# Kernel optimization log

Measured on AMD Instinct MI355X. Metric: run time of the kernel, lower is better.

## Reference

```python
import jax, jax.numpy as jnp
import numpy as np

L, H, E, HS, T, B, V = 6, 12, 768, 64, 1024, 2, 32000
EPS = 1e-5


def layer_norm(x, g, b):
    mu = jnp.mean(x, axis=-1, keepdims=True)
    var = jnp.mean(jnp.square(x - mu), axis=-1, keepdims=True)
    return (x - mu) * jax.lax.rsqrt(var + EPS) * g + b


def setup_inputs() -> dict:
    key = jax.random.key(0)
    ks = jax.random.split(key, 24)
    s = 0.02
    inp = {
        "idx": jax.random.randint(ks[0], (B, T), 0, V),
        "targets": jax.random.randint(ks[1], (B, T), 0, V),
        "tok_emb": jax.random.normal(ks[2], (V, E), jnp.float32) * s,
        "pos_emb": jax.random.normal(ks[3], (T, E), jnp.float32) * s,
        "ln1_g": jnp.ones((L, E), jnp.float32),
        "ln1_b": jnp.zeros((L, E), jnp.float32),
        "wq": jax.random.normal(ks[4], (L, E, E), jnp.float32) * s,
        "wk": jax.random.normal(ks[5], (L, E, E), jnp.float32) * s,
        "wv": jax.random.normal(ks[6], (L, E, E), jnp.float32) * s,
        "wproj": jax.random.normal(ks[7], (L, E, E), jnp.float32) * s,
        "bproj": jnp.zeros((L, E), jnp.float32),
        "ln2_g": jnp.ones((L, E), jnp.float32),
        "ln2_b": jnp.zeros((L, E), jnp.float32),
        "w1": jax.random.normal(ks[8], (L, E, 4 * E), jnp.float32) * s,
        "b1": jnp.zeros((L, 4 * E), jnp.float32),
        "w2": jax.random.normal(ks[9], (L, 4 * E, E), jnp.float32) * s,
        "b2": jnp.zeros((L, E), jnp.float32),
        "lnf_g": jnp.ones((E,), jnp.float32),
        "lnf_b": jnp.zeros((E,), jnp.float32),
        "lm_w": jax.random.normal(ks[10], (E, V), jnp.float32) * s,
        "lm_b": jnp.zeros((V,), jnp.float32),
    }
    return inp


def reference(idx, targets, tok_emb, pos_emb, ln1_g, ln1_b, wq, wk, wv, wproj,
              bproj, ln2_g, ln2_b, w1, b1, w2, b2, lnf_g, lnf_b, lm_w, lm_b):
    x = tok_emb[idx] + pos_emb[None, :T, :]  # [B,T,E]
    causal = jnp.tril(jnp.ones((T, T), bool))
    scale = E ** (-0.5)  # NOTE: original scales by n_embed**-0.5, not head_size
    for l in range(L):
        h = layer_norm(x, ln1_g[l], ln1_b[l])
        q = (h @ wq[l]).reshape(B, T, H, HS)
        k = (h @ wk[l]).reshape(B, T, H, HS)
        v = (h @ wv[l]).reshape(B, T, H, HS)
        scores = jnp.einsum('bqhd,bkhd->bhqk', q, k) * scale
        scores = jnp.where(causal[None, None], scores, -jnp.inf)
        w = jax.nn.softmax(scores, axis=-1)
        attn = jnp.einsum('bhqk,bkhd->bqhd', w, v).reshape(B, T, E)
        # original MultiHeadAttention applies proj TWICE (faithful reproduction)
        out = attn @ wproj[l] + bproj[l]
        out = out @ wproj[l] + bproj[l]
        x = x + out
        h2 = layer_norm(x, ln2_g[l], ln2_b[l])
        x = x + (jax.nn.relu(h2 @ w1[l] + b1[l]) @ w2[l] + b2[l])
    x = layer_norm(x, lnf_g, lnf_b)
    logits = x @ lm_w + lm_b  # [B,T,V]
    logp = jax.nn.log_softmax(logits, axis=-1)
    nll = -jnp.take_along_axis(logp, targets[..., None], axis=-1)[..., 0]
    loss = jnp.mean(nll)
    return logits, loss
```

## Files before the change

kernel.cpp:

```cpp
#include <hip/hip_runtime.h>
#include <math.h>

#define NL 6
#define NH 12
#define NE 768
#define NHS 64
#define NT 1024
#define NB 2
#define NV 32000
#define NM (NB * NT)
#define NQKV (3 * NE)
#define NFF (4 * NE)
#define LN_EPS 1e-5f

typedef __attribute__((ext_vector_type(8))) short short8;
typedef __attribute__((ext_vector_type(4))) float f32x4;
typedef __attribute__((ext_vector_type(4))) unsigned short ushort4v;
typedef __attribute__((address_space(1))) const unsigned int as1_cuint;
typedef __attribute__((address_space(3))) unsigned int as3_uint;

__device__ __forceinline__ unsigned short f2bf(float f) {
    unsigned int u = __builtin_bit_cast(unsigned int, f);
    u += 0x7fffu + ((u >> 16) & 1u);
    return (unsigned short)(u >> 16);
}
__device__ __forceinline__ float bf2f(unsigned short u) {
    unsigned int v = ((unsigned int)u) << 16;
    return __builtin_bit_cast(float, v);
}
__device__ __forceinline__ void gload_lds16(const void* g, void* l) {
    __builtin_amdgcn_global_load_lds((as1_cuint*)g, (as3_uint*)l, 16, 0, 0);
}

__global__ __launch_bounds__(256) void embed_ln_kernel(const int* __restrict__ idx,
                                                       const float* __restrict__ tok,
                                                       const float* __restrict__ pos,
                                                       const float* __restrict__ g,
                                                       const float* __restrict__ b,
                                                       float* __restrict__ x,
                                                       unsigned short* __restrict__ hbuf) {
    __shared__ float red[256];
    int row = blockIdx.x, tid = threadIdx.x;
    int t = row % NT;
    int id = idx[row];
    float v[3]; float s = 0.f;
    #pragma unroll
    for (int k = 0; k < 3; ++k) {
        int c = tid + k * 256;
        v[k] = tok[(long)id * NE + c] + pos[(long)t * NE + c];
        x[(long)row * NE + c] = v[k];
        s += v[k];
    }
    red[tid] = s; __syncthreads();
    for (int o = 128; o > 0; o >>= 1) { if (tid < o) red[tid] += red[tid + o]; __syncthreads(); }
    float mu = red[0] / NE;
    __syncthreads();
    float vr = 0.f;
    #pragma unroll
    for (int k = 0; k < 3; ++k) { float d = v[k] - mu; vr += d * d; }
    red[tid] = vr; __syncthreads();
    for (int o = 128; o > 0; o >>= 1) { if (tid < o) red[tid] += red[tid + o]; __syncthreads(); }
    float rstd = rsqrtf(red[0] / NE + LN_EPS);
    #pragma unroll
    for (int k = 0; k < 3; ++k) {
        int c = tid + k * 256;
        hbuf[(long)row * NE + c] = f2bf((v[k] - mu) * rstd * g[c] + b[c]);
    }
}

template<int S>
__global__ __launch_bounds__(256) void combine_ln_kernel(const float* __restrict__ parts,
                                                         const float* __restrict__ bias,
                                                         float* __restrict__ x,
                                                         const float* __restrict__ g,
                                                         const float* __restrict__ b,
                                                         unsigned short* __restrict__ hbuf) {
    __shared__ float red[256];
    int row = blockIdx.x, tid = threadIdx.x;
    float v[3]; float s = 0.f;
    #pragma unroll
    for (int k = 0; k < 3; ++k) {
        int c = tid + k * 256;
        long i = (long)row * NE + c;
        float a = parts[i];
        #pragma unroll
        for (int si = 1; si < S; ++si) a += parts[(long)si * NM * NE + i];
        a += bias[c] + x[i];
        x[i] = a;
        v[k] = a; s += a;
    }
    red[tid] = s; __syncthreads();
    for (int o = 128; o > 0; o >>= 1) { if (tid < o) red[tid] += red[tid + o]; __syncthreads(); }
    float mu = red[0] / NE;
    __syncthreads();
    float vr = 0.f;
    #pragma unroll
    for (int k = 0; k < 3; ++k) { float d = v[k] - mu; vr += d * d; }
    red[tid] = vr; __syncthreads();
    for (int o = 128; o > 0; o >>= 1) { if (tid < o) red[tid] += red[tid + o]; __syncthreads(); }
    float rstd = rsqrtf(red[0] / NE + LN_EPS);
    #pragma unroll
    for (int k = 0; k < 3; ++k) {
        int c = tid + k * 256;
        hbuf[(long)row * NE + c] = f2bf((v[k] - mu) * rstd * g[c] + b[c]);
    }
}

__global__ __launch_bounds__(256) void transpose4b_kernel(const float* __restrict__ wq,
                                                          const float* __restrict__ wk,
                                                          const float* __restrict__ wv,
                                                          const float* __restrict__ wp,
                                                          unsigned short* __restrict__ wqkvT,
                                                          unsigned short* __restrict__ wprojT) {
    __shared__ float t[32][33];
    int z = blockIdx.z, l = z >> 2, which = z & 3;
    const float* W = ((which == 0) ? wq : (which == 1) ? wk : (which == 2) ? wv : wp) + (long)l * NE * NE;
    unsigned short* WT = (which < 3) ? (wqkvT + (long)l * NQKV * NE + (long)which * NE * NE)
                                     : (wprojT + (long)l * NE * NE);
    int k0 = blockIdx.y * 32, n0 = blockIdx.x * 32;
    int c = threadIdx.x & 31, r = threadIdx.x >> 5;
    #pragma unroll
    for (int p = 0; p < 4; ++p)
        t[r + p * 8][c] = W[(long)(k0 + r + p * 8) * NE + n0 + c];
    __syncthreads();
    #pragma unroll
    for (int p = 0; p < 4; ++p)
        WT[(long)(n0 + r + p * 8) * NE + k0 + c] = f2bf(t[c][r + p * 8]);
}

__global__ __launch_bounds__(256) void transpose_cast_b_kernel(const float* __restrict__ W0,
                                                               unsigned short* __restrict__ WT0,
                                                               int K, int N) {
    __shared__ float t[32][33];
    long lofs = (long)blockIdx.z * K * N;
    const float* W = W0 + lofs;
    unsigned short* WT = WT0 + lofs;
    int k0 = blockIdx.y * 32, n0 = blockIdx.x * 32;
    int c = threadIdx.x & 31, r = threadIdx.x >> 5;
    #pragma unroll
    for (int p = 0; p < 4; ++p)
        t[r + p * 8][c] = W[(long)(k0 + r + p * 8) * N + n0 + c];
    __syncthreads();
    #pragma unroll
    for (int p = 0; p < 4; ++p)
        WT[(long)(n0 + r + p * 8) * K + k0 + c] = f2bf(t[c][r + p * 8]);
}

__global__ __launch_bounds__(256) void cast_kernel(const float* __restrict__ W,
                                                   unsigned short* __restrict__ O, long n) {
    long i = ((long)blockIdx.x * 256 + threadIdx.x) * 4;
    if (i < n) {
        float4 v = *(const float4*)(W + i);
        ushort4v o;
        o[0] = f2bf(v.x); o[1] = f2bf(v.y); o[2] = f2bf(v.z); o[3] = f2bf(v.w);
        *(ushort4v*)(O + i) = o;
    }
}

__global__ __launch_bounds__(256) void beff_b_kernel(const float* __restrict__ bproj,
                                                     const unsigned short* __restrict__ wprojT,
                                                     float* __restrict__ beff) {
    __shared__ float red[256];
    int n = blockIdx.x, l = blockIdx.y, tid = threadIdx.x;
    const unsigned short* wp = wprojT + (long)l * NE * NE + (long)n * NE;
    const float* bp = bproj + (long)l * NE;
    float acc = 0.f;
    for (int j = tid; j < NE; j += 256) acc += bp[j] * bf2f(wp[j]);
    red[tid] = acc; __syncthreads();
    for (int o = 128; o > 0; o >>= 1) { if (tid < o) red[tid] += red[tid + o]; __syncthreads(); }
    if (tid == 0) beff[(long)l * NE + n] = red[0] + bp[n];
}

template<int S>
__global__ __launch_bounds__(256) void combine_kernel(const float* __restrict__ parts,
                                                      unsigned short* __restrict__ bout,
                                                      long total) {
    long i = ((long)blockIdx.x * 256 + threadIdx.x) * 4;
    if (i >= total) return;
    float4 a = *(const float4*)(parts + i);
    #pragma unroll
    for (int s = 1; s < S; ++s) {
        float4 b = *(const float4*)(parts + (long)s * total + i);
        a.x += b.x; a.y += b.y; a.z += b.z; a.w += b.w;
    }
    ushort4v o;
    o[0] = f2bf(a.x); o[1] = f2bf(a.y); o[2] = f2bf(a.z); o[3] = f2bf(a.w);
    *(ushort4v*)(bout + i) = o;
}

template<typename OutT, bool BIAS, bool RELU, int SPLITK>
__global__ __launch_bounds__(256) void gemm_mfma(const unsigned short* __restrict__ A,
                                                 const unsigned short* __restrict__ BT,
                                                 const float* __restrict__ bias,
                                                 OutT* __restrict__ C,
                                                 int gridM, int N, int K) {
    __shared__ unsigned short As[3][128 * 32];
    __shared__ unsigned short Bs[3][128 * 32];
    int tid = threadIdx.x;
    int lane = tid & 63, w = tid >> 6;
    int wr = w >> 1, wc = w & 1;
    int l4 = lane >> 4, l15 = lane & 15;

    int nwg = gridDim.x, orig = blockIdx.x;
    int q = nwg >> 3, r8 = nwg & 7;
    int xcd = orig & 7, ii = orig >> 3;
    int wg = (xcd < r8) ? (xcd * (q + 1) + ii) : (r8 * (q + 1) + (xcd - r8) * q + ii);
    int bm = wg % gridM, bn = wg / gridM;
    int m0 = bm * 128, n0 = bn * 128;

    int kb = K / SPLITK;
    int koff = (SPLITK > 1) ? blockIdx.y * kb : 0;
    int nkt = kb >> 5;

    f32x4 acc[4][4] = {};

    int srow = lane >> 2;
    int scol = ((lane & 3) ^ ((lane >> 3) & 3)) * 8;
    int rsw  = (l4 ^ ((l15 >> 1) & 3)) * 8;

    auto STAGE = [&](int slot, int kt) {
        #pragma unroll
        for (int it = 0; it < 2; ++it) {
            int rr = w * 32 + it * 16;
            gload_lds16(&A [(long)(m0 + rr + srow) * K + koff + kt * 32 + scol], &As[slot][rr * 32]);
            gload_lds16(&BT[(long)(n0 + rr + srow) * K + koff + kt * 32 + scol], &Bs[slot][rr * 32]);
        }
    };

    STAGE(0, 0);
    if (nkt > 1) STAGE(1, 1);

    int s = 0;
    for (int t = 0; t < nkt; ++t) {
        if (t + 2 < nkt) STAGE((t + 2) % 3, t + 2);
        int ahead = nkt - 1 - t;
        if (ahead >= 2)      asm volatile("s_waitcnt vmcnt(8)" ::: "memory");
        else if (ahead == 1) asm volatile("s_waitcnt vmcnt(4)" ::: "memory");
        else                 asm volatile("s_waitcnt vmcnt(0)" ::: "memory");
        asm volatile("s_barrier" ::: "memory");

        short8 a[4], b[4];
        #pragma unroll
        for (int f = 0; f < 4; ++f) {
            a[f] = *(const short8*)&As[s][(wr * 64 + f * 16 + l15) * 32 + rsw];
            b[f] = *(const short8*)&Bs[s][(wc * 64 + f * 16 + l15) * 32 + rsw];
        }
        asm volatile("s_waitcnt lgkmcnt(0)" ::: "memory");
        asm volatile("s_barrier" ::: "memory");

        __builtin_amdgcn_s_setprio(1);
        #pragma unroll
        for (int fm = 0; fm < 4; ++fm)
            #pragma unroll
            for (int fn = 0; fn < 4; ++fn)
                acc[fm][fn] = __builtin_amdgcn_mfma_f32_16x16x32_bf16(a[fm], b[fn], acc[fm][fn], 0, 0, 0);
        __builtin_amdgcn_s_setprio(0);
        s = (s + 1) % 3;
    }

    if constexpr (SPLITK > 1) {
        float* Cp = (float*)C + (long)blockIdx.y * gridM * 128 * N;
        #pragma unroll
        for (int fm = 0; fm < 4; ++fm)
            #pragma unroll
            for (int j = 0; j < 4; ++j) {
                long row = m0 + wr * 64 + fm * 16 + l4 * 4 + j;
                #pragma unroll
                for (int fn = 0; fn < 4; ++fn)
                    Cp[row * N + n0 + wc * 64 + fn * 16 + l15] = acc[fm][fn][j];
            }
    } else {
        float bs[4];
        #pragma unroll
        for (int fn = 0; fn < 4; ++fn)
            bs[fn] = BIAS ? bias[n0 + wc * 64 + fn * 16 + l15] : 0.f;

        #pragma unroll
        for (int fm = 0; fm < 4; ++fm) {
            #pragma unroll
            for (int j = 0; j < 4; ++j) {
                long row = m0 + wr * 64 + fm * 16 + l4 * 4 + j;
                #pragma unroll
                for (int fn = 0; fn < 4; ++fn) {
                    int col = n0 + wc * 64 + fn * 16 + l15;
                    float v = acc[fm][fn][j] + bs[fn];
                    if (RELU) v = fmaxf(v, 0.f);
                    if constexpr (sizeof(OutT) == 2) C[row * N + col] = (OutT)f2bf(v);
                    else                             C[row * N + col] = v;
                }
            }
        }
    }
}

__global__ __launch_bounds__(256) void gemm_weff_kernel(const unsigned short* __restrict__ A0,
                                                        const unsigned short* __restrict__ B0,
                                                        unsigned short* __restrict__ C0,
                                                        int gridM, int N, int K) {
    __shared__ unsigned short As[2][128 * 32];
    __shared__ unsigned short Bs[2][128 * 32];
    long zofs = (long)blockIdx.z * N * K;
    const unsigned short* A = A0 + zofs;
    const unsigned short* BT = B0 + zofs;
    unsigned short* C = C0 + zofs;
    int tid = threadIdx.x;
    int lane = tid & 63, w = tid >> 6;
    int wr = w >> 1, wc = w & 1;
    int l4 = lane >> 4, l15 = lane & 15;
    int bm = blockIdx.x % gridM, bn = blockIdx.x / gridM;
    int m0 = bm * 128, n0 = bn * 128;

    f32x4 acc[4][4] = {};
    int srow = lane >> 2;
    int scol = ((lane & 3) ^ ((lane >> 3) & 3)) * 8;
    int rsw  = (l4 ^ ((l15 >> 1) & 3)) * 8;

    #pragma unroll
    for (int it = 0; it < 2; ++it) {
        int rr = w * 32 + it * 16;
        gload_lds16(&A [(long)(m0 + rr + srow) * K + scol], &As[0][rr * 32]);
        gload_lds16(&BT[(long)(n0 + rr + srow) * K + scol], &Bs[0][rr * 32]);
    }
    int cur = 0;
    for (int k0 = 0; k0 < K; k0 += 32) {
        __syncthreads();
        if (k0 + 32 < K) {
            #pragma unroll
            for (int it = 0; it < 2; ++it) {
                int rr = w * 32 + it * 16;
                gload_lds16(&A [(long)(m0 + rr + srow) * K + k0 + 32 + scol], &As[cur ^ 1][rr * 32]);
                gload_lds16(&BT[(long)(n0 + rr + srow) * K + k0 + 32 + scol], &Bs[cur ^ 1][rr * 32]);
            }
        }
        short8 a[4], b[4];
        #pragma unroll
        for (int f = 0; f < 4; ++f) {
            a[f] = *(const short8*)&As[cur][(wr * 64 + f * 16 + l15) * 32 + rsw];
            b[f] = *(const short8*)&Bs[cur][(wc * 64 + f * 16 + l15) * 32 + rsw];
        }
        #pragma unroll
        for (int fm = 0; fm < 4; ++fm)
            #pragma unroll
            for (int fn = 0; fn < 4; ++fn)
                acc[fm][fn] = __builtin_amdgcn_mfma_f32_16x16x32_bf16(a[fm], b[fn], acc[fm][fn], 0, 0, 0);
        cur ^= 1;
    }
    #pragma unroll
    for (int fm = 0; fm < 4; ++fm)
        #pragma unroll
        for (int j = 0; j < 4; ++j) {
            long row = m0 + wr * 64 + fm * 16 + l4 * 4 + j;
            #pragma unroll
            for (int fn = 0; fn < 4; ++fn)
                C[row * N + n0 + wc * 64 + fn * 16 + l15] = f2bf(acc[fm][fn][j]);
        }
}

__global__ __launch_bounds__(512, 4) void gemm256x128_lse(const unsigned short* __restrict__ A,
                                                          const unsigned short* __restrict__ BT,
                                                          const float* __restrict__ bias,
                                                          float* __restrict__ C,
                                                          float* __restrict__ pm, float* __restrict__ ps,
                                                          int gridM, int N, int K) {
    __shared__ unsigned short Al[3][256 * 32];
    __shared__ unsigned short Bl[3][128 * 32];
    int tid = threadIdx.x;
    int lane = tid & 63, w = tid >> 6;
    int wm = w >> 1, wn = w & 1;
    int l4 = lane >> 4, l15 = lane & 15;

    int nwg = gridDim.x, orig = blockIdx.x;
    int q = nwg >> 3, r8 = nwg & 7;
    int xcd = orig & 7, ii = orig >> 3;
    int wg = (xcd < r8) ? (xcd * (q + 1) + ii) : (r8 * (q + 1) + (xcd - r8) * q + ii);
    int bm = wg % gridM, bn = wg / gridM;
    int m0 = bm * 256, n0 = bn * 128;

    int nkt = K >> 5;
    int srow = lane >> 2;
    int sslot = ((lane & 3) ^ ((lane >> 3) & 3)) * 8;

    auto STAGE = [&](int slot, int kt) {
        #pragma unroll
        for (int p = 0; p < 2; ++p) {
            int r0 = p * 128 + w * 16;
            gload_lds16(&A[(long)(m0 + r0 + srow) * K + kt * 32 + sslot], &Al[slot][r0 * 32]);
        }
        int r0 = w * 16;
        gload_lds16(&BT[(long)(n0 + r0 + srow) * K + kt * 32 + sslot], &Bl[slot][r0 * 32]);
    };

    f32x4 acc[4][4] = {};
    int rsw = (l4 ^ ((l15 >> 1) & 3)) * 8;

    STAGE(0, 0);
    STAGE(1, 1);
    int s = 0;
    for (int t = 0; t < nkt; ++t) {
        if (t + 2 < nkt) STAGE((t + 2) % 3, t + 2);
        int ahead = nkt - 1 - t;
        if (ahead >= 2)      asm volatile("s_waitcnt vmcnt(6)" ::: "memory");
        else if (ahead == 1) asm volatile("s_waitcnt vmcnt(3)" ::: "memory");
        else                 asm volatile("s_waitcnt vmcnt(0)" ::: "memory");
        asm volatile("s_barrier" ::: "memory");

        short8 af[4], bf[4];
        #pragma unroll
        for (int f = 0; f < 4; ++f) {
            af[f] = *(const short8*)&Al[s][(wm * 64 + f * 16 + l15) * 32 + rsw];
            bf[f] = *(const short8*)&Bl[s][(wn * 64 + f * 16 + l15) * 32 + rsw];
        }
        asm volatile("s_waitcnt lgkmcnt(0)" ::: "memory");
        asm volatile("s_barrier" ::: "memory");

        __builtin_amdgcn_s_setprio(1);
        #pragma unroll
        for (int fm = 0; fm < 4; ++fm)
            #pragma unroll
            for (int fn = 0; fn < 4; ++fn)
                acc[fm][fn] = __builtin_amdgcn_mfma_f32_16x16x32_bf16(af[fm], bf[fn], acc[fm][fn], 0, 0, 0);
        __builtin_amdgcn_s_setprio(0);
        s = (s + 1) % 3;
    }

    float bs[4];
    #pragma unroll
    for (int fn = 0; fn < 4; ++fn)
        bs[fn] = bias[n0 + wn * 64 + fn * 16 + l15];

    #pragma unroll
    for (int fm = 0; fm < 4; ++fm) {
        #pragma unroll
        for (int j = 0; j < 4; ++j) {
            long row = m0 + wm * 64 + fm * 16 + l4 * 4 + j;
            float v4[4];
            #pragma unroll
            for (int fn = 0; fn < 4; ++fn) {
                int col = n0 + wn * 64 + fn * 16 + l15;
                float v = acc[fm][fn][j] + bs[fn];
                __builtin_nontemporal_store(v, &C[row * N + col]);
                v4[fn] = v;
            }
            float mx = fmaxf(fmaxf(v4[0], v4[1]), fmaxf(v4[2], v4[3]));
            #pragma unroll
            for (int off = 1; off < 16; off <<= 1) mx = fmaxf(mx, __shfl_xor(mx, off));
            float sm = 0.f;
            #pragma unroll
            for (int fn = 0; fn < 4; ++fn) sm += __expf(v4[fn] - mx);
            #pragma unroll
            for (int off = 1; off < 16; off <<= 1) sm += __shfl_xor(sm, off);
            if (l15 == 0) {
                int pidx = bn * 2 + wn;
                pm[row * 512 + pidx] = mx;
                ps[row * 512 + pidx] = sm;
            }
        }
    }
}

__global__ __launch_bounds__(256) void vtrans_kernel(const unsigned short* __restrict__ qkv,
                                                     unsigned short* __restrict__ vt) {
    __shared__ unsigned short t[64][72];
    int t0 = blockIdx.x * 64;
    int bh = blockIdx.y;
    int b = bh / NH, h = bh % NH;
    int tid = threadIdx.x;
    #pragma unroll
    for (int i = 0; i < 2; ++i) {
        int r = (tid >> 3) + i * 32, c8 = (tid & 7) * 8;
        short8 v = *(const short8*)(qkv + ((long)b * NT + t0 + r) * NQKV + 2 * NE + h * NHS + c8);
        *(short8*)&t[r][c8] = v;
    }
    __syncthreads();
    #pragma unroll
    for (int i = 0; i < 2; ++i) {
        int d = (tid >> 3) + i * 32, s = (tid & 7) * 8;
        short8 o;
        #pragma unroll
        for (int j = 0; j < 8; ++j) o[j] = (short)t[s + j][d];
        *(short8*)(vt + ((long)bh * NHS + d) * NT + t0 + s) = o;
    }
}

__global__ __launch_bounds__(256) void fattn_kernel(const unsigned short* __restrict__ qkv,
                                                    const unsigned short* __restrict__ vt,
                                                    unsigned short* __restrict__ out) {
    __shared__ unsigned short Ks[2][64 * 64];
    __shared__ unsigned short Vl[2][64 * 64];
    __shared__ unsigned short Ps[4 * 16 * 64];
    int qt = gridDim.x - 1 - blockIdx.x;
    int bh = blockIdx.y;
    int b = bh / NH, h = bh % NH;
    int tid = threadIdx.x, lane = tid & 63, w = tid >> 6;
    int l4 = lane >> 4, l15 = lane & 15;
    long rowb = (long)b * NT;
    const float scale = 0.03608439182435161f;
    const unsigned short* vtp = vt + (long)bh * NHS * NT;

    const unsigned short* qptr = qkv + (rowb + qt * 64 + w * 16 + l15) * NQKV + h * NHS;
    short8 qa0 = *(const short8*)(qptr + l4 * 8);
    short8 qa1 = *(const short8*)(qptr + 32 + l4 * 8);

    f32x4 o[4] = {};
    float m[4], lsum[4];
    #pragma unroll
    for (int j = 0; j < 4; ++j) { m[j] = -INFINITY; lsum[j] = 0.f; }

    int kr_r = tid >> 3, kr_c = (tid & 7) * 8;
    int vr_d = tid >> 3, vr_s = tid & 7;

    short8 kr[2], vr[2];
    auto LOADT = [&](int t) {
        int kbase = t * 64;
        #pragma unroll
        for (int i = 0; i < 2; ++i) {
            kr[i] = *(const short8*)(qkv + (rowb + kbase + kr_r + i * 32) * NQKV + NE + h * NHS + kr_c);
            vr[i] = *(const short8*)(vtp + (long)(vr_d + i * 32) * NT + kbase + vr_s * 8);
        }
    };

    LOADT(0);
    for (int t = 0; t <= qt; ++t) {
        int cur = t & 1;
        #pragma unroll
        for (int i = 0; i < 2; ++i) {
            int r = kr_r + i * 32;
            *(short8*)&Ks[cur][r * 64 + (kr_c ^ ((r & 7) << 3))] = kr[i];
            int d = vr_d + i * 32;
            *(short8*)&Vl[cur][d * 64 + ((vr_s * 8) ^ ((d & 7) << 3))] = vr[i];
        }
        asm volatile("s_waitcnt lgkmcnt(0)" ::: "memory");
        if (t < qt) LOADT(t + 1);
        asm volatile("s_barrier" ::: "memory");

        f32x4 s[4];
        __builtin_amdgcn_s_setprio(1);
        #pragma unroll
        for (int fn = 0; fn < 4; ++fn) {
            int key = fn * 16 + l15;
            short8 kb0 = *(const short8*)&Ks[cur][key * 64 + ((l4 * 8) ^ ((key & 7) << 3))];
            short8 kb1 = *(const short8*)&Ks[cur][key * 64 + ((32 + l4 * 8) ^ ((key & 7) << 3))];
            f32x4 z = {};
            z = __builtin_amdgcn_mfma_f32_16x16x32_bf16(qa0, kb0, z, 0, 0, 0);
            s[fn] = __builtin_amdgcn_mfma_f32_16x16x32_bf16(qa1, kb1, z, 0, 0, 0);
        }
        __builtin_amdgcn_s_setprio(0);

        if (t == qt) {
            #pragma unroll
            for (int fn = 0; fn < 4; ++fn) {
                int key = t * 64 + fn * 16 + l15;
                #pragma unroll
                for (int j = 0; j < 4; ++j) {
                    int qrow = qt * 64 + w * 16 + l4 * 4 + j;
                    s[fn][j] = (key <= qrow) ? s[fn][j] * scale : -1e30f;
                }
            }
        } else {
            #pragma unroll
            for (int fn = 0; fn < 4; ++fn)
                #pragma unroll
                for (int j = 0; j < 4; ++j)
                    s[fn][j] *= scale;
        }

        #pragma unroll
        for (int j = 0; j < 4; ++j) {
            float mj = fmaxf(fmaxf(s[0][j], s[1][j]), fmaxf(s[2][j], s[3][j]));
            #pragma unroll
            for (int off = 1; off < 16; off <<= 1) mj = fmaxf(mj, __shfl_xor(mj, off));
            float mnew = fmaxf(m[j], mj);
            float alpha = __expf(m[j] - mnew);
            m[j] = mnew;
            float psum = 0.f;
            #pragma unroll
            for (int fn = 0; fn < 4; ++fn) {
                float p = __expf(s[fn][j] - mnew);
                psum += p;
                int rr = l4 * 4 + j, c = fn * 16 + l15;
                Ps[w * 1024 + rr * 64 + (c ^ ((rr & 7) << 3))] = f2bf(p);
            }
            #pragma unroll
            for (int off = 1; off < 16; off <<= 1) psum += __shfl_xor(psum, off);
            lsum[j] = lsum[j] * alpha + psum;
            #pragma unroll
            for (int fn = 0; fn < 4; ++fn) o[fn][j] *= alpha;
        }

        short8 pa0 = *(const short8*)&Ps[w * 1024 + l15 * 64 + ((l4 * 8) ^ ((l15 & 7) << 3))];
        short8 pa1 = *(const short8*)&Ps[w * 1024 + l15 * 64 + ((32 + l4 * 8) ^ ((l15 & 7) << 3))];
        __builtin_amdgcn_s_setprio(1);
        #pragma unroll
        for (int fn = 0; fn < 4; ++fn) {
            int d = fn * 16 + l15;
            short8 vb0 = *(const short8*)&Vl[cur][d * 64 + ((l4 * 8) ^ ((d & 7) << 3))];
            short8 vb1 = *(const short8*)&Vl[cur][d * 64 + ((32 + l4 * 8) ^ ((d & 7) << 3))];
            o[fn] = __builtin_amdgcn_mfma_f32_16x16x32_bf16(pa0, vb0, o[fn], 0, 0, 0);
            o[fn] = __builtin_amdgcn_mfma_f32_16x16x32_bf16(pa1, vb1, o[fn], 0, 0, 0);
        }
        __builtin_amdgcn_s_setprio(0);
    }

    #pragma unroll
    for (int j = 0; j < 4; ++j) {
        long row = rowb + qt * 64 + w * 16 + l4 * 4 + j;
        float inv = 1.0f / lsum[j];
        #pragma unroll
        for (int fn = 0; fn < 4; ++fn)
            out[row * NE + h * NHS + fn * 16 + l15] = f2bf(o[fn][j] * inv);
    }
}

__global__ __launch_bounds__(256) void nll_combine_kernel(const float* __restrict__ logits,
                                                          const float* __restrict__ pm,
                                                          const float* __restrict__ ps,
                                                          const int* __restrict__ targets,
                                                          float* __restrict__ nll) {
    __shared__ float rm[256], rs[256];
    int row = blockIdx.x, tid = threadIdx.x;
    float m = -1e30f, s = 0.f;
    for (int i = tid; i < 500; i += 256) {
        float m2 = pm[(long)row * 512 + i], s2 = ps[(long)row * 512 + i];
        float mm = fmaxf(m, m2);
        s = s * __expf(m - mm) + s2 * __expf(m2 - mm);
        m = mm;
    }
    rm[tid] = m; rs[tid] = s; __syncthreads();
    for (int o = 128; o > 0; o >>= 1) {
        if (tid < o) {
            float m2 = rm[tid + o], s2 = rs[tid + o];
            float mm = fmaxf(rm[tid], m2);
            rs[tid] = rs[tid] * __expf(rm[tid] - mm) + s2 * __expf(m2 - mm);
            rm[tid] = mm;
        }
        __syncthreads();
    }
    if (tid == 0) {
        int tgt = targets[row];
        nll[row] = -(logits[(long)row * NV + tgt] - rm[0] - logf(rs[0]));
    }
}

__global__ void loss_reduce_kernel(const float* __restrict__ nll, float* __restrict__ out) {
    __shared__ float red[256];
    int tid = threadIdx.x;
    float s = 0.f;
    for (int i = tid; i < NM; i += 256) s += nll[i];
    red[tid] = s; __syncthreads();
    for (int o = 128; o > 0; o >>= 1) { if (tid < o) red[tid] += red[tid + o]; __syncthreads(); }
    if (tid == 0) out[0] = red[0] / NM;
}

extern "C" void kernel_launch(void* const* d_in, const int* in_sizes, int n_in,
                              void* d_out, int out_size, void* d_ws, size_t ws_size,
                              hipStream_t stream) {
    const int*   idx     = (const int*)  d_in[0];
    const int*   targets = (const int*)  d_in[1];
    const float* tok     = (const float*)d_in[2];
    const float* pos     = (const float*)d_in[3];
    const float* ln1_g   = (const float*)d_in[4];
    const float* ln1_b   = (const float*)d_in[5];
    const float* wq      = (const float*)d_in[6];
    const float* wk      = (const float*)d_in[7];
    const float* wv      = (const float*)d_in[8];
    const float* wproj   = (const float*)d_in[9];
    const float* bproj   = (const float*)d_in[10];
    const float* ln2_g   = (const float*)d_in[11];
    const float* ln2_b   = (const float*)d_in[12];
    const float* w1      = (const float*)d_in[13];
    const float* b1      = (const float*)d_in[14];
    const float* w2      = (const float*)d_in[15];
    const float* b2      = (const float*)d_in[16];
    const float* lnf_g   = (const float*)d_in[17];
    const float* lnf_b   = (const float*)d_in[18];
    const float* lm_w    = (const float*)d_in[19];
    const float* lm_b    = (const float*)d_in[20];

    float* logits = (float*)d_out;
    float* loss   = logits + (long)NM * NV;

    char* p = (char*)d_ws;
    float*          x      = (float*)p;          p += (long)NM * NE * 4;
    unsigned short* hbuf   = (unsigned short*)p; p += (long)NM * NE * 2;
    unsigned short* qkv    = (unsigned short*)p; p += (long)NM * NQKV * 2;
    unsigned short* att    = (unsigned short*)p; p += (long)NM * NE * 2;
    unsigned short* hid    = (unsigned short*)p; p += (long)NM * NFF * 2;
    unsigned short* vt     = (unsigned short*)p; p += (long)NB * NH * NHS * NT * 2;
    float*          nll    = (float*)p;          p += (long)NM * 4;
    float*          pmb    = (float*)p;          p += (long)NM * 512 * 4;
    float*          psb    = (float*)p;          p += (long)NM * 512 * 4;
    float*          parts  = (float*)p;          p += (long)2 * NM * NQKV * 4;
    unsigned short* wqkvT6 = (unsigned short*)p; p += (long)NL * NQKV * NE * 2;
    unsigned short* wprojT6= (unsigned short*)p; p += (long)NL * NE * NE * 2;
    unsigned short* wprojC6= (unsigned short*)p; p += (long)NL * NE * NE * 2;
    unsigned short* weffT6 = (unsigned short*)p; p += (long)NL * NE * NE * 2;
    float*          beff6  = (float*)p;          p += (long)NL * NE * 4;
    unsigned short* w1T6   = (unsigned short*)p; p += (long)NL * NFF * NE * 2;
    unsigned short* w2T6   = (unsigned short*)p; p += (long)NL * NE * NFF * 2;
    unsigned short* lmT    = (unsigned short*)p; p += (long)NV * NE * 2;

    dim3 blk(256);

    transpose4b_kernel<<<dim3(NE / 32, NE / 32, 4 * NL), blk, 0, stream>>>(
        wq, wk, wv, wproj, wqkvT6, wprojT6);
    cast_kernel<<<(NL * NE * NE) / 1024, blk, 0, stream>>>(wproj, wprojC6, (long)NL * NE * NE);
    transpose_cast_b_kernel<<<dim3(NFF / 32, NE / 32, NL), blk, 0, stream>>>(w1, w1T6, NE, NFF);
    transpose_cast_b_kernel<<<dim3(NE / 32, NFF / 32, NL), blk, 0, stream>>>(w2, w2T6, NFF, NE);
    gemm_weff_kernel<<<dim3(36, 1, NL), blk, 0, stream>>>(wprojT6, wprojC6, weffT6, 6, NE, NE);
    beff_b_kernel<<<dim3(NE, NL), blk, 0, stream>>>(bproj, wprojT6, beff6);
    transpose_cast_b_kernel<<<dim3(NV / 32, NE / 32, 1), blk, 0, stream>>>(lm_w, lmT, NE, NV);

    embed_ln_kernel<<<NM, blk, 0, stream>>>(idx, tok, pos, ln1_g, ln1_b, x, hbuf);

    for (int l = 0; l < NL; ++l) {
        gemm_mfma<float, false, false, 2><<<dim3((NM/128)*(NQKV/128), 2), blk, 0, stream>>>(
            hbuf, wqkvT6 + (long)l * NQKV * NE, nullptr, parts, NM / 128, NQKV, NE);
        combine_kernel<2><<<(NM * NQKV) / 1024, blk, 0, stream>>>(parts, qkv, (long)NM * NQKV);
        vtrans_kernel<<<dim3(NT / 64, NB * NH), blk, 0, stream>>>(qkv, vt);
        fattn_kernel<<<dim3(NT / 64, NB * NH), blk, 0, stream>>>(qkv, vt, att);
        gemm_mfma<float, false, false, 2><<<dim3((NM/128)*(NE/128), 2), blk, 0, stream>>>(
            att, weffT6 + (long)l * NE * NE, nullptr, parts, NM / 128, NE, NE);
        combine_ln_kernel<2><<<NM, blk, 0, stream>>>(
            parts, beff6 + (long)l * NE, x, ln2_g + (long)l * NE, ln2_b + (long)l * NE, hbuf);
        gemm_mfma<unsigned short, true, true, 1><<<dim3((NM/128)*(NFF/128)), blk, 0, stream>>>(
            hbuf, w1T6 + (long)l * NFF * NE, b1 + (long)l * NFF, hid, NM / 128, NFF, NE);
        gemm_mfma<float, false, false, 4><<<dim3((NM/128)*(NE/128), 4), blk, 0, stream>>>(
            hid, w2T6 + (long)l * NE * NFF, nullptr, parts, NM / 128, NE, NFF);
        const float* ng = (l < NL - 1) ? (ln1_g + (long)(l + 1) * NE) : lnf_g;
        const float* nb = (l < NL - 1) ? (ln1_b + (long)(l + 1) * NE) : lnf_b;
        combine_ln_kernel<4><<<NM, blk, 0, stream>>>(parts, b2 + (long)l * NE, x, ng, nb, hbuf);
    }

    gemm256x128_lse<<<dim3((NM/256)*(NV/128)), dim3(512), 0, stream>>>(
        hbuf, lmT, lm_b, logits, pmb, psb, NM / 256, NV, NE);
    nll_combine_kernel<<<NM, blk, 0, stream>>>(logits, pmb, psb, targets, nll);
    loss_reduce_kernel<<<1, blk, 0, stream>>>(nll, loss);
}
```

Baseline: 1.140 ms.

## Widen attention query tile to 128 rows and drop split-K for QKV GEMM

The flash-attention kernel now runs 512 threads (8 waves) per block over 128 query rows, so each loaded K/V tile is shared by twice as many queries, and each thread loads one K and one V vector per tile instead of two. The causal mask now applies to the last two key tiles. Separately, the QKV projection GEMM runs without split-K and writes bf16 output directly, which removes the fp32 partials buffer and the combine kernel launch. The costs are half as many attention blocks with more causal-imbalanced work per block, and fewer workgroups for the QKV GEMM.

```diff
diff --git a/kernel.cpp b/kernel.cpp
--- a/kernel.cpp
+++ b/kernel.cpp
@@ -169,23 +169,6 @@
     red[tid] = acc; __syncthreads();
     for (int o = 128; o > 0; o >>= 1) { if (tid < o) red[tid] += red[tid + o]; __syncthreads(); }
     if (tid == 0) beff[(long)l * NE + n] = red[0] + bp[n];
-}
-
-template<int S>
-__global__ __launch_bounds__(256) void combine_kernel(const float* __restrict__ parts,
-                                                      unsigned short* __restrict__ bout,
-                                                      long total) {
-    long i = ((long)blockIdx.x * 256 + threadIdx.x) * 4;
-    if (i >= total) return;
-    float4 a = *(const float4*)(parts + i);
-    #pragma unroll
-    for (int s = 1; s < S; ++s) {
-        float4 b = *(const float4*)(parts + (long)s * total + i);
-        a.x += b.x; a.y += b.y; a.z += b.z; a.w += b.w;
-    }
-    ushort4v o;
-    o[0] = f2bf(a.x); o[1] = f2bf(a.y); o[2] = f2bf(a.z); o[3] = f2bf(a.w);
-    *(ushort4v*)(bout + i) = o;
 }
 
 template<typename OutT, bool BIAS, bool RELU, int SPLITK>
@@ -482,12 +465,12 @@
     }
 }
 
-__global__ __launch_bounds__(256) void fattn_kernel(const unsigned short* __restrict__ qkv,
+__global__ __launch_bounds__(512) void fattn_kernel(const unsigned short* __restrict__ qkv,
                                                     const unsigned short* __restrict__ vt,
                                                     unsigned short* __restrict__ out) {
     __shared__ unsigned short Ks[2][64 * 64];
     __shared__ unsigned short Vl[2][64 * 64];
-    __shared__ unsigned short Ps[4 * 16 * 64];
+    __shared__ unsigned short Ps[8 * 16 * 64];
     int qt = gridDim.x - 1 - blockIdx.x;
     int bh = blockIdx.y;
     int b = bh / NH, h = bh % NH;
@@ -497,7 +480,7 @@
     const float scale = 0.03608439182435161f;
     const unsigned short* vtp = vt + (long)bh * NHS * NT;
 
-    const unsigned short* qptr = qkv + (rowb + qt * 64 + w * 16 + l15) * NQKV + h * NHS;
+    const unsigned short* qptr = qkv + (rowb + qt * 128 + w * 16 + l15) * NQKV + h * NHS;
     short8 qa0 = *(const short8*)(qptr + l4 * 8);
     short8 qa1 = *(const short8*)(qptr + 32 + l4 * 8);
 
@@ -509,28 +492,21 @@
     int kr_r = tid >> 3, kr_c = (tid & 7) * 8;
     int vr_d = tid >> 3, vr_s = tid & 7;
 
-    short8 kr[2], vr[2];
+    short8 kr, vr;
     auto LOADT = [&](int t) {
         int kbase = t * 64;
-        #pragma unroll
-        for (int i = 0; i < 2; ++i) {
-            kr[i] = *(const short8*)(qkv + (rowb + kbase + kr_r + i * 32) * NQKV + NE + h * NHS + kr_c);
-            vr[i] = *(const short8*)(vtp + (long)(vr_d + i * 32) * NT + kbase + vr_s * 8);
-        }
+        kr = *(const short8*)(qkv + (rowb + kbase + kr_r) * NQKV + NE + h * NHS + kr_c);
+        vr = *(const short8*)(vtp + (long)vr_d * NT + kbase + vr_s * 8);
     };
 
+    int ntiles = 2 * qt + 2;
     LOADT(0);
-    for (int t = 0; t <= qt; ++t) {
+    for (int t = 0; t < ntiles; ++t) {
         int cur = t & 1;
-        #pragma unroll
-        for (int i = 0; i < 2; ++i) {
-            int r = kr_r + i * 32;
-            *(short8*)&Ks[cur][r * 64 + (kr_c ^ ((r & 7) << 3))] = kr[i];
-            int d = vr_d + i * 32;
-            *(short8*)&Vl[cur][d * 64 + ((vr_s * 8) ^ ((d & 7) << 3))] = vr[i];
-        }
+        *(short8*)&Ks[cur][kr_r * 64 + (kr_c ^ ((kr_r & 7) << 3))] = kr;
+        *(short8*)&Vl[cur][vr_d * 64 + ((vr_s * 8) ^ ((vr_d & 7) << 3))] = vr;
         asm volatile("s_waitcnt lgkmcnt(0)" ::: "memory");
-        if (t < qt) LOADT(t + 1);
+        if (t + 1 < ntiles) LOADT(t + 1);
         asm volatile("s_barrier" ::: "memory");
 
         f32x4 s[4];
@@ -546,13 +522,13 @@
         }
         __builtin_amdgcn_s_setprio(0);
 
-        if (t == qt) {
+        if (t >= 2 * qt) {
             #pragma unroll
             for (int fn = 0; fn < 4; ++fn) {
                 int key = t * 64 + fn * 16 + l15;
                 #pragma unroll
                 for (int j = 0; j < 4; ++j) {
-                    int qrow = qt * 64 + w * 16 + l4 * 4 + j;
+                    int qrow = qt * 128 + w * 16 + l4 * 4 + j;
                     s[fn][j] = (key <= qrow) ? s[fn][j] * scale : -1e30f;
                 }
             }
@@ -603,7 +579,7 @@
 
     #pragma unroll
     for (int j = 0; j < 4; ++j) {
-        long row = rowb + qt * 64 + w * 16 + l4 * 4 + j;
+        long row = rowb + qt * 128 + w * 16 + l4 * 4 + j;
         float inv = 1.0f / lsum[j];
         #pragma unroll
         for (int fn = 0; fn < 4; ++fn)
@@ -713,11 +689,10 @@
     embed_ln_kernel<<<NM, blk, 0, stream>>>(idx, tok, pos, ln1_g, ln1_b, x, hbuf);
 
     for (int l = 0; l < NL; ++l) {
-        gemm_mfma<float, false, false, 2><<<dim3((NM/128)*(NQKV/128), 2), blk, 0, stream>>>(
-            hbuf, wqkvT6 + (long)l * NQKV * NE, nullptr, parts, NM / 128, NQKV, NE);
-        combine_kernel<2><<<(NM * NQKV) / 1024, blk, 0, stream>>>(parts, qkv, (long)NM * NQKV);
+        gemm_mfma<unsigned short, false, false, 1><<<dim3((NM/128)*(NQKV/128)), blk, 0, stream>>>(
+            hbuf, wqkvT6 + (long)l * NQKV * NE, nullptr, qkv, NM / 128, NQKV, NE);
         vtrans_kernel<<<dim3(NT / 64, NB * NH), blk, 0, stream>>>(qkv, vt);
-        fattn_kernel<<<dim3(NT / 64, NB * NH), blk, 0, stream>>>(qkv, vt, att);
+        fattn_kernel<<<dim3(NT / 128, NB * NH), dim3(512), 0, stream>>>(qkv, vt, att);
         gemm_mfma<float, false, false, 2><<<dim3((NM/128)*(NE/128), 2), blk, 0, stream>>>(
             att, weffT6 + (long)l * NE * NE, nullptr, parts, NM / 128, NE, NE);
         combine_ln_kernel<2><<<NM, blk, 0, stream>>>(
```

Result: faster. 1.087 ms (-4.6%).
